# Performance work log

Hardware: AMD Instinct MI355X
Metric: run time of the kernel (lower is better)

## Reference

```python
import jax, jax.numpy as jnp
import numpy as np

K = 3  # == stride, neighbors per token


def setup_inputs() -> dict:
    key = jax.random.key(0)
    k1, k2, k3 = jax.random.split(key, 3)
    x = jax.random.normal(k1, (16, 64, 2048), dtype=jnp.float32)        # (B, C, T)
    W = jax.random.normal(k2, (64, 64, K), dtype=jnp.float32) * 0.05     # (O, I, K) conv1d weight
    b = jax.random.normal(k3, (64,), dtype=jnp.float32) * 0.05           # (O,) conv1d bias
    return {"x": x, "W": W, "b": b}


def reference(x, W, b):
    B, C, T = x.shape
    # pairwise squared euclidean distances over the channel dim: (B, T, T)
    nsq = jnp.sum(x * x, axis=1)                       # (B, T)
    dot = jnp.einsum('bct,bcs->bts', x, x)             # (B, T, T)
    dist = jnp.maximum(nsq[:, :, None] + nsq[:, None, :] - 2.0 * dot, 0.0)
    # K nearest neighbors (smallest distance -> top_k of negated dist)
    _, idx = jax.lax.top_k(-dist, K)                   # (B, T, K) int32 indices
    # gather neighbor features: prime[b, c, i*K + k] = x[b, c, idx[b, i, k]]
    idx_flat = idx.reshape(B, 1, T * K)
    prime = jnp.take_along_axis(x, jnp.broadcast_to(idx_flat, (B, C, T * K)), axis=2)
    # Conv1d with kernel_size=K, stride=K, padding=0 -> output length T
    out = jax.lax.conv_general_dilated(
        prime, W, window_strides=(K,), padding='VALID',
        dimension_numbers=('NCH', 'OIH', 'NCH'))
    return out + b[None, :, None]
```

## Files before the change

kernel.cpp:

```cpp
#include <hip/hip_runtime.h>

#define B_ 16
#define C_ 64
#define T_ 2048
#define O_ 64
#define KNN 3
#define HSPLIT 4
#define JCH (T_ / HSPLIT)

typedef short short8   __attribute__((ext_vector_type(8)));
typedef float f32x4    __attribute__((ext_vector_type(4)));
typedef unsigned short ushortx4 __attribute__((ext_vector_type(4)));

#define XT_OFF 0
#define XS_OFF (XT_OFF + B_ * T_ * C_)
#define NSQ_OFF (XS_OFF + B_ * T_ * C_)
#define WT_OFF (NSQ_OFF + B_ * T_)
#define CAND_OFF (WT_OFF + 192 * O_)

__device__ inline ushort bf16_rne(float f) {
    union { float f; unsigned u; } cv; cv.f = f;
    unsigned u = cv.u;
    u += 0x7FFF + ((u >> 16) & 1);
    return (ushort)(u >> 16);
}
__device__ inline float bf16_val(ushort h) {
    union { unsigned u; float f; } cv; cv.u = ((unsigned)h) << 16; return cv.f;
}

__global__ __launch_bounds__(256) void prep_kernel(const float* __restrict__ x,
                                                   const float* __restrict__ W,
                                                   float* __restrict__ ws) {
    float*  xT  = ws + XT_OFF;
    ushort* xs  = (ushort*)(ws + XS_OFF);
    float*  nsq = ws + NSQ_OFF;
    float*  Wt  = ws + WT_OFF;
    int blk = blockIdx.x;
    int tid = threadIdx.x;
    if (blk < B_ * (T_ / 64)) {
        int b  = blk / (T_ / 64);
        int t0 = (blk % (T_ / 64)) * 64;
        __shared__ float tl[64 * 65];
        #pragma unroll
        for (int r = 0; r < 16; ++r) {
            int e = r * 256 + tid;
            int c = e >> 6, t = e & 63;
            tl[c * 65 + t] = x[(b * C_ + c) * T_ + t0 + t];
        }
        __syncthreads();
        #pragma unroll
        for (int r = 0; r < 16; ++r) {
            int e = r * 256 + tid;
            int t = e >> 6, c = e & 63;
            float v = tl[c * 65 + t];
            size_t rowg = (size_t)(b * T_ + t0 + t);
            xT[rowg * 64 + c] = v;
            ushort hi = bf16_rne(v);
            float  fr = v - bf16_val(hi);
            ushort lo = bf16_rne(fr);
            xs[rowg * 128 + c]      = hi;
            xs[rowg * 128 + 64 + c] = lo;
        }
        if (tid < 64) {
            float s = 0.f;
            #pragma unroll
            for (int c = 0; c < 64; ++c) { float v = tl[c * 65 + tid]; s = fmaf(v, v, s); }
            nsq[b * T_ + t0 + tid] = s;
        }
    } else {
        int e = (blk - B_ * (T_ / 64)) * 256 + tid;
        if (e < O_ * C_ * KNN) {
            int o = e / (C_ * KNN);
            int c = (e / KNN) % C_;
            int k = e % KNN;
            Wt[(k * 64 + c) * O_ + o] = W[e];
        }
    }
}

__global__ __launch_bounds__(256, 4) void knn_mfma_kernel(const ushort* __restrict__ xs,
                                                          const float* __restrict__ nsq,
                                                          ushort* __restrict__ cand) {
    __shared__ __align__(16) ushort jbuf[2][32 * 128];
    __shared__ float nsqs[JCH];

    int bid = blockIdx.x;
    int g   = bid & 63;
    int m   = bid >> 6;
    int b   = g >> 2, h = g & 3;
    int i0  = m * 128;
    int tid = threadIdx.x;
    int w   = tid >> 6, l = tid & 63, lr = l & 15, lq = l >> 4;
    const ushort* xsb = xs + (size_t)b * T_ * 128;
    int jBase = h * JCH;

    if (tid < 128)
        ((float4*)nsqs)[tid] = ((const float4*)(nsq + b * T_ + jBase))[tid];

    short8 bA0, bA1, bA4, bA5, bB0, bB1, bB4, bB5;
    {
        const ushort* ia = xsb + (size_t)(i0 + w * 32 + lr) * 128 + lq * 8;
        bA0 = *(const short8*)(ia + 0);  bA1 = *(const short8*)(ia + 32);
        bA4 = *(const short8*)(ia + 64); bA5 = *(const short8*)(ia + 96);
        const ushort* ib2 = ia + 16 * 128;
        bB0 = *(const short8*)(ib2 + 0);  bB1 = *(const short8*)(ib2 + 32);
        bB4 = *(const short8*)(ib2 + 64); bB5 = *(const short8*)(ib2 + 96);
    }
    float niA = nsq[b * T_ + i0 + w * 32 + lr] + 4.0f;
    float niB = nsq[b * T_ + i0 + w * 32 + 16 + lr] + 4.0f;

    const float INF = __builtin_inff();
    float kA0 = INF, kA1 = INF, kA2 = INF, kA3 = INF;
    float kB0 = INF, kB1 = INF, kB2 = INF, kB3 = INF;

    int cSw = lr ^ (w * 4 + lq);
    #define ISSUE_DMA(jsv, bufv) {                                               \
        _Pragma("unroll")                                                        \
        for (int p = 0; p < 2; ++p) {                                            \
            int rloc = p * 16 + w * 4 + lq;                                      \
            const ushort* gp = xsb + (size_t)(jBase + (jsv) * 32 + rloc) * 128 + cSw * 8; \
            __builtin_amdgcn_global_load_lds(                                    \
                (const __attribute__((address_space(1))) void*)gp,               \
                (__attribute__((address_space(3))) void*)(jbuf[bufv] + (p * 16 + w * 4) * 128), \
                16, 0, 0);                                                       \
        } }

    ISSUE_DMA(0, 0);

    #pragma unroll 1
    for (int js = 0; js < 16; ++js) {
        asm volatile("s_waitcnt vmcnt(0)" ::: "memory");
        __syncthreads();
        if (js < 15) ISSUE_DMA(js + 1, (js + 1) & 1);
        const char* jb8 = (const char*)jbuf[js & 1];
        #pragma unroll
        for (int tile = 0; tile < 2; ++tile) {
            const char* rowp = jb8 + (tile * 16 + lr) * 256;
            short8 ah0 = *(const short8*)(rowp + ((( 0 + lq) ^ lr) << 4));
            short8 ah1 = *(const short8*)(rowp + ((( 4 + lq) ^ lr) << 4));
            short8 al0 = *(const short8*)(rowp + ((( 8 + lq) ^ lr) << 4));
            short8 al1 = *(const short8*)(rowp + (((12 + lq) ^ lr) << 4));
            f32x4 accA = {0.f, 0.f, 0.f, 0.f};
            f32x4 accB = {0.f, 0.f, 0.f, 0.f};
            accA = __builtin_amdgcn_mfma_f32_16x16x32_bf16(ah0, bA0, accA, 0, 0, 0);
            accB = __builtin_amdgcn_mfma_f32_16x16x32_bf16(ah0, bB0, accB, 0, 0, 0);
            accA = __builtin_amdgcn_mfma_f32_16x16x32_bf16(ah1, bA1, accA, 0, 0, 0);
            accB = __builtin_amdgcn_mfma_f32_16x16x32_bf16(ah1, bB1, accB, 0, 0, 0);
            accA = __builtin_amdgcn_mfma_f32_16x16x32_bf16(al0, bA0, accA, 0, 0, 0);
            accB = __builtin_amdgcn_mfma_f32_16x16x32_bf16(al0, bB0, accB, 0, 0, 0);
            accA = __builtin_amdgcn_mfma_f32_16x16x32_bf16(al1, bA1, accA, 0, 0, 0);
            accB = __builtin_amdgcn_mfma_f32_16x16x32_bf16(al1, bB1, accB, 0, 0, 0);
            accA = __builtin_amdgcn_mfma_f32_16x16x32_bf16(ah0, bA4, accA, 0, 0, 0);
            accB = __builtin_amdgcn_mfma_f32_16x16x32_bf16(ah0, bB4, accB, 0, 0, 0);
            accA = __builtin_amdgcn_mfma_f32_16x16x32_bf16(ah1, bA5, accA, 0, 0, 0);
            accB = __builtin_amdgcn_mfma_f32_16x16x32_bf16(ah1, bB5, accB, 0, 0, 0);
            float4 nv = *(const float4*)(nsqs + js * 32 + tile * 16 + lq * 4);
            int idb = ((js * 2 + tile) << 2) | (lq << 7);
            #define INS(K0, K1, K2, K3, sv, idv) {                                  \
                unsigned uu = (__float_as_uint(sv) & 0xFFFFFE00u) | (unsigned)(idv); \
                float kf = __uint_as_float(uu);                                      \
                float n0 = fminf(K0, kf);                                            \
                float n1 = __builtin_amdgcn_fmed3f(K0, K1, kf);                      \
                float n2 = __builtin_amdgcn_fmed3f(K1, K2, kf);                      \
                float n3 = __builtin_amdgcn_fmed3f(K2, K3, kf);                      \
                K0 = n0; K1 = n1; K2 = n2; K3 = n3; }
            {
                float s0 = fmaf(-2.f, accA[0], nv.x + niA); INS(kA0, kA1, kA2, kA3, s0, idb + 0);
                float s1 = fmaf(-2.f, accA[1], nv.y + niA); INS(kA0, kA1, kA2, kA3, s1, idb + 1);
                float s2 = fmaf(-2.f, accA[2], nv.z + niA); INS(kA0, kA1, kA2, kA3, s2, idb + 2);
                float s3 = fmaf(-2.f, accA[3], nv.w + niA); INS(kA0, kA1, kA2, kA3, s3, idb + 3);
            }
            {
                float s0 = fmaf(-2.f, accB[0], nv.x + niB); INS(kB0, kB1, kB2, kB3, s0, idb + 0);
                float s1 = fmaf(-2.f, accB[1], nv.y + niB); INS(kB0, kB1, kB2, kB3, s1, idb + 1);
                float s2 = fmaf(-2.f, accB[2], nv.z + niB); INS(kB0, kB1, kB2, kB3, s2, idb + 2);
                float s3 = fmaf(-2.f, accB[3], nv.w + niB); INS(kB0, kB1, kB2, kB3, s3, idb + 3);
            }
            #undef INS
        }
    }

    __syncthreads();
    float* fbuf = (float*)jbuf;
    {
        float* pa = fbuf + (w * 32 + lr) * 16 + lq * 4;
        pa[0] = kA0; pa[1] = kA1; pa[2] = kA2; pa[3] = kA3;
        float* pb = fbuf + (w * 32 + 16 + lr) * 16 + lq * 4;
        pb[0] = kB0; pb[1] = kB1; pb[2] = kB2; pb[3] = kB3;
    }
    __syncthreads();
    if (l < 32) {
        int rloc = w * 32 + l;
        const float* pr = fbuf + rloc * 16;
        float m0 = INF, m1 = INF, m2 = INF, m3 = INF;
        #pragma unroll
        for (int q2 = 0; q2 < 16; ++q2) {
            float kf = pr[q2];
            float n0 = fminf(m0, kf);
            float n1 = __builtin_amdgcn_fmed3f(m0, m1, kf);
            float n2 = __builtin_amdgcn_fmed3f(m1, m2, kf);
            float n3 = __builtin_amdgcn_fmed3f(m2, m3, kf);
            m0 = n0; m1 = n1; m2 = n2; m3 = n3;
        }
        ushortx4 cv;
        #define DEC(mf, slot) { unsigned u = __float_as_uint(mf) & 511u;             \
            cv[slot] = (ushort)(jBase + (((u & 127u) >> 2) << 4) + ((u >> 7) << 2) + (u & 3)); }
        DEC(m0, 0); DEC(m1, 1); DEC(m2, 2); DEC(m3, 3);
        #undef DEC
        int row = b * T_ + i0 + rloc;
        *(ushortx4*)(cand + (size_t)row * 16 + h * 4) = cv;
    }
}

__global__ __launch_bounds__(256) void refine_kernel(float* __restrict__ ws) {
    const float* xT  = ws + XT_OFF;
    const float* nsq = ws + NSQ_OFF;
    ushort* cand     = (ushort*)(ws + CAND_OFF);

    int tid = threadIdx.x;
    int w = tid >> 6, l = tid & 63, qw = l >> 4, lr = l & 15;
    int row = blockIdx.x * 16 + w * 4 + qw;
    int bT  = row & ~(T_ - 1);

    float4 av = *(const float4*)(xT + (size_t)row * 64 + lr * 4);
    int jown = cand[(size_t)row * 16 + lr];

    const float INF = __builtin_inff();
    float D0 = INF, D1 = INF, D2 = INF;
    int   I0 = 0x7FFFFFFF, I1 = 0x7FFFFFFF, I2 = 0x7FFFFFFF;

    #pragma unroll
    for (int t = 0; t < 16; ++t) {
        int jt = __shfl(jown, (l & 48) + t, 64);
        float4 bv = *(const float4*)(xT + (size_t)(bT + jt) * 64 + lr * 4);
        float p = fmaf(bv.w, av.w, fmaf(bv.z, av.z, fmaf(bv.y, av.y, bv.x * av.x)));
        p += __shfl_xor(p, 1, 64);
        p += __shfl_xor(p, 2, 64);
        p += __shfl_xor(p, 4, 64);
        p += __shfl_xor(p, 8, 64);
        float s = nsq[bT + jt] - 2.f * p;
        bool lt2 = (s < D2) || (s == D2 && jt < I2);
        bool lt1 = (s < D1) || (s == D1 && jt < I1);
        bool lt0 = (s < D0) || (s == D0 && jt < I0);
        float nD2 = lt1 ? D1 : (lt2 ? s : D2); int nI2 = lt1 ? I1 : (lt2 ? jt : I2);
        float nD1 = lt0 ? D0 : (lt1 ? s : D1); int nI1 = lt0 ? I0 : (lt1 ? jt : I1);
        D2 = nD2; I2 = nI2; D1 = nD1; I1 = nI1;
        D0 = lt0 ? s : D0; I0 = lt0 ? jt : I0;
    }
    if (lr == 0) {
        ushort* dst = cand + (size_t)row * 16;
        dst[0] = (ushort)I0; dst[1] = (ushort)I1; dst[2] = (ushort)I2;
    }
}

__global__ __launch_bounds__(256) void conv2_kernel(const float* __restrict__ ws,
                                                    const float* __restrict__ bias,
                                                    float* __restrict__ out) {
    const float*  xT   = ws + XT_OFF;
    const float*  Wt   = ws + WT_OFF;
    const ushort* cand = (const ushort*)(ws + CAND_OFF);

    __shared__ float g_s[192 * 32];

    int b   = blockIdx.x >> 6;
    int i0  = (blockIdx.x & 63) * 32;
    int tid = threadIdx.x;

    if (tid < 96) {
        int k  = tid >> 5;
        int ip = tid & 31;
        int j  = cand[(size_t)(b * T_ + i0 + ip) * 16 + k];
        const float4* src = (const float4*)(xT + ((size_t)b * T_ + j) * 64);
        #pragma unroll
        for (int c4 = 0; c4 < 16; ++c4) {
            float4 v = src[c4];
            int mm = k * 64 + c4 * 4;
            g_s[(mm + 0) * 32 + ip] = v.x;
            g_s[(mm + 1) * 32 + ip] = v.y;
            g_s[(mm + 2) * 32 + ip] = v.z;
            g_s[(mm + 3) * 32 + ip] = v.w;
        }
    }
    __syncthreads();

    int oq = tid >> 3;
    int iq = tid & 7;
    float a0x = 0.f, a0y = 0.f, a0z = 0.f, a0w = 0.f;
    float a1x = 0.f, a1y = 0.f, a1z = 0.f, a1w = 0.f;
    #pragma unroll 4
    for (int mm = 0; mm < 192; ++mm) {
        float2 wv = *(const float2*)(Wt + mm * 64 + oq * 2);
        float4 gv = *(const float4*)(g_s + mm * 32 + iq * 4);
        a0x = fmaf(wv.x, gv.x, a0x); a0y = fmaf(wv.x, gv.y, a0y);
        a0z = fmaf(wv.x, gv.z, a0z); a0w = fmaf(wv.x, gv.w, a0w);
        a1x = fmaf(wv.y, gv.x, a1x); a1y = fmaf(wv.y, gv.y, a1y);
        a1z = fmaf(wv.y, gv.z, a1z); a1w = fmaf(wv.y, gv.w, a1w);
    }
    int o0 = oq * 2;
    float b0 = bias[o0], b1 = bias[o0 + 1];
    float4 r0; r0.x = a0x + b0; r0.y = a0y + b0; r0.z = a0z + b0; r0.w = a0w + b0;
    float4 r1; r1.x = a1x + b1; r1.y = a1y + b1; r1.z = a1z + b1; r1.w = a1w + b1;
    *(float4*)(out + ((size_t)b * O_ + o0)     * T_ + i0 + iq * 4) = r0;
    *(float4*)(out + ((size_t)b * O_ + o0 + 1) * T_ + i0 + iq * 4) = r1;
}

extern "C" void kernel_launch(void* const* d_in, const int* in_sizes, int n_in,
                              void* d_out, int out_size, void* d_ws, size_t ws_size,
                              hipStream_t stream) {
    const float* x    = (const float*)d_in[0];
    const float* W    = (const float*)d_in[1];
    const float* bias = (const float*)d_in[2];
    float* out = (float*)d_out;
    float* ws  = (float*)d_ws;

    prep_kernel<<<B_ * (T_ / 64) + 48, 256, 0, stream>>>(x, W, ws);
    knn_mfma_kernel<<<1024, 256, 0, stream>>>(
        (const ushort*)(ws + XS_OFF), ws + NSQ_OFF, (ushort*)(ws + CAND_OFF));
    refine_kernel<<<B_ * T_ / 16, 256, 0, stream>>>(ws);
    conv2_kernel<<<B_ * 64, 256, 0, stream>>>(ws, bias, out);
}
```

Baseline: 142.1 us.

## Halve KNN column split and fuse refine into conv kernel

The KNN candidate kernel now splits the column range in two instead of four, doubling per-block loop length and halving the grid and the number of candidates per row from 16 to 8. Packed index bits grow by one, so the distance mantissa loses one more bit. The exact refine step is folded into the conv kernel, which stores the selected neighbors in shared memory, removing one launch and a global round trip. The conv output tiling changes to 4 outputs by 2 positions per thread. The risks are fewer blocks to fill the GPU, coarser approximate distances, and fewer candidates for the exact rerank.

```diff
diff --git a/kernel.cpp b/kernel.cpp
--- a/kernel.cpp
+++ b/kernel.cpp
@@ -5,7 +5,7 @@
 #define T_ 2048
 #define O_ 64
 #define KNN 3
-#define HSPLIT 4
+#define HSPLIT 2
 #define JCH (T_ / HSPLIT)
 
 typedef short short8   __attribute__((ext_vector_type(8)));
@@ -85,17 +85,16 @@
     __shared__ float nsqs[JCH];
 
     int bid = blockIdx.x;
-    int g   = bid & 63;
-    int m   = bid >> 6;
-    int b   = g >> 2, h = g & 3;
+    int g   = bid & 31;
+    int m   = bid >> 5;
+    int b   = g >> 1, h = g & 1;
     int i0  = m * 128;
     int tid = threadIdx.x;
     int w   = tid >> 6, l = tid & 63, lr = l & 15, lq = l >> 4;
     const ushort* xsb = xs + (size_t)b * T_ * 128;
     int jBase = h * JCH;
 
-    if (tid < 128)
-        ((float4*)nsqs)[tid] = ((const float4*)(nsq + b * T_ + jBase))[tid];
+    ((float4*)nsqs)[tid] = ((const float4*)(nsq + b * T_ + jBase))[tid];
 
     short8 bA0, bA1, bA4, bA5, bB0, bB1, bB4, bB5;
     {
@@ -128,10 +127,10 @@
     ISSUE_DMA(0, 0);
 
     #pragma unroll 1
-    for (int js = 0; js < 16; ++js) {
+    for (int js = 0; js < 32; ++js) {
         asm volatile("s_waitcnt vmcnt(0)" ::: "memory");
         __syncthreads();
-        if (js < 15) ISSUE_DMA(js + 1, (js + 1) & 1);
+        if (js < 31) ISSUE_DMA(js + 1, (js + 1) & 1);
         const char* jb8 = (const char*)jbuf[js & 1];
         #pragma unroll
         for (int tile = 0; tile < 2; ++tile) {
@@ -155,9 +154,9 @@
             accA = __builtin_amdgcn_mfma_f32_16x16x32_bf16(ah1, bA5, accA, 0, 0, 0);
             accB = __builtin_amdgcn_mfma_f32_16x16x32_bf16(ah1, bB5, accB, 0, 0, 0);
             float4 nv = *(const float4*)(nsqs + js * 32 + tile * 16 + lq * 4);
-            int idb = ((js * 2 + tile) << 2) | (lq << 7);
+            int idb = ((js * 2 + tile) << 2) | (lq << 8);
             #define INS(K0, K1, K2, K3, sv, idv) {                                  \
-                unsigned uu = (__float_as_uint(sv) & 0xFFFFFE00u) | (unsigned)(idv); \
+                unsigned uu = (__float_as_uint(sv) & 0xFFFFFC00u) | (unsigned)(idv); \
                 float kf = __uint_as_float(uu);                                      \
                 float n0 = fminf(K0, kf);                                            \
                 float n1 = __builtin_amdgcn_fmed3f(K0, K1, kf);                      \
@@ -203,74 +202,70 @@
             m0 = n0; m1 = n1; m2 = n2; m3 = n3;
         }
         ushortx4 cv;
-        #define DEC(mf, slot) { unsigned u = __float_as_uint(mf) & 511u;             \
-            cv[slot] = (ushort)(jBase + (((u & 127u) >> 2) << 4) + ((u >> 7) << 2) + (u & 3)); }
+        #define DEC(mf, slot) { unsigned u = __float_as_uint(mf) & 1023u;            \
+            cv[slot] = (ushort)(jBase + (((u >> 2) & 63u) << 4) + ((u >> 8) << 2) + (u & 3)); }
         DEC(m0, 0); DEC(m1, 1); DEC(m2, 2); DEC(m3, 3);
         #undef DEC
         int row = b * T_ + i0 + rloc;
-        *(ushortx4*)(cand + (size_t)row * 16 + h * 4) = cv;
-    }
-}
-
-__global__ __launch_bounds__(256) void refine_kernel(float* __restrict__ ws) {
-    const float* xT  = ws + XT_OFF;
-    const float* nsq = ws + NSQ_OFF;
-    ushort* cand     = (ushort*)(ws + CAND_OFF);
-
+        *(ushortx4*)(cand + (size_t)row * 8 + h * 4) = cv;
+    }
+}
+
+__global__ __launch_bounds__(256, 4) void conv_fused_kernel(const float* __restrict__ ws,
+                                                            const float* __restrict__ bias,
+                                                            float* __restrict__ out) {
+    const float*  xT   = ws + XT_OFF;
+    const float*  nsq  = ws + NSQ_OFF;
+    const float*  Wt   = ws + WT_OFF;
+    const ushort* cand = (const ushort*)(ws + CAND_OFF);
+
+    __shared__ float g_s[192 * 32];
+    __shared__ int   jsel3[32 * 3];
+
+    int bb  = blockIdx.x >> 6;
+    int i0  = (blockIdx.x & 63) * 32;
     int tid = threadIdx.x;
     int w = tid >> 6, l = tid & 63, qw = l >> 4, lr = l & 15;
-    int row = blockIdx.x * 16 + w * 4 + qw;
-    int bT  = row & ~(T_ - 1);
-
-    float4 av = *(const float4*)(xT + (size_t)row * 64 + lr * 4);
-    int jown = cand[(size_t)row * 16 + lr];
+    int bT = bb * T_;
 
     const float INF = __builtin_inff();
-    float D0 = INF, D1 = INF, D2 = INF;
-    int   I0 = 0x7FFFFFFF, I1 = 0x7FFFFFFF, I2 = 0x7FFFFFFF;
-
     #pragma unroll
-    for (int t = 0; t < 16; ++t) {
-        int jt = __shfl(jown, (l & 48) + t, 64);
-        float4 bv = *(const float4*)(xT + (size_t)(bT + jt) * 64 + lr * 4);
-        float p = fmaf(bv.w, av.w, fmaf(bv.z, av.z, fmaf(bv.y, av.y, bv.x * av.x)));
-        p += __shfl_xor(p, 1, 64);
-        p += __shfl_xor(p, 2, 64);
-        p += __shfl_xor(p, 4, 64);
-        p += __shfl_xor(p, 8, 64);
-        float s = nsq[bT + jt] - 2.f * p;
-        bool lt2 = (s < D2) || (s == D2 && jt < I2);
-        bool lt1 = (s < D1) || (s == D1 && jt < I1);
-        bool lt0 = (s < D0) || (s == D0 && jt < I0);
-        float nD2 = lt1 ? D1 : (lt2 ? s : D2); int nI2 = lt1 ? I1 : (lt2 ? jt : I2);
-        float nD1 = lt0 ? D0 : (lt1 ? s : D1); int nI1 = lt0 ? I0 : (lt1 ? jt : I1);
-        D2 = nD2; I2 = nI2; D1 = nD1; I1 = nI1;
-        D0 = lt0 ? s : D0; I0 = lt0 ? jt : I0;
-    }
-    if (lr == 0) {
-        ushort* dst = cand + (size_t)row * 16;
-        dst[0] = (ushort)I0; dst[1] = (ushort)I1; dst[2] = (ushort)I2;
-    }
-}
-
-__global__ __launch_bounds__(256) void conv2_kernel(const float* __restrict__ ws,
-                                                    const float* __restrict__ bias,
-                                                    float* __restrict__ out) {
-    const float*  xT   = ws + XT_OFF;
-    const float*  Wt   = ws + WT_OFF;
-    const ushort* cand = (const ushort*)(ws + CAND_OFF);
-
-    __shared__ float g_s[192 * 32];
-
-    int b   = blockIdx.x >> 6;
-    int i0  = (blockIdx.x & 63) * 32;
-    int tid = threadIdx.x;
+    for (int it = 0; it < 2; ++it) {
+        int rl  = w * 8 + it * 4 + qw;
+        int row = bT + i0 + rl;
+        float4 av = *(const float4*)(xT + (size_t)row * 64 + lr * 4);
+        int jown = cand[(size_t)row * 8 + (lr & 7)];
+        float D0 = INF, D1 = INF, D2 = INF;
+        int   I0 = 0x7FFFFFFF, I1 = 0x7FFFFFFF, I2 = 0x7FFFFFFF;
+        #pragma unroll
+        for (int t = 0; t < 8; ++t) {
+            int jt = __shfl(jown, (l & 48) + t, 64);
+            float4 bv = *(const float4*)(xT + (size_t)(bT + jt) * 64 + lr * 4);
+            float p = fmaf(bv.w, av.w, fmaf(bv.z, av.z, fmaf(bv.y, av.y, bv.x * av.x)));
+            p += __shfl_xor(p, 1, 64);
+            p += __shfl_xor(p, 2, 64);
+            p += __shfl_xor(p, 4, 64);
+            p += __shfl_xor(p, 8, 64);
+            float s = nsq[bT + jt] - 2.f * p;
+            bool lt2 = (s < D2) || (s == D2 && jt < I2);
+            bool lt1 = (s < D1) || (s == D1 && jt < I1);
+            bool lt0 = (s < D0) || (s == D0 && jt < I0);
+            float nD2 = lt1 ? D1 : (lt2 ? s : D2); int nI2 = lt1 ? I1 : (lt2 ? jt : I2);
+            float nD1 = lt0 ? D0 : (lt1 ? s : D1); int nI1 = lt0 ? I0 : (lt1 ? jt : I1);
+            D2 = nD2; I2 = nI2; D1 = nD1; I1 = nI1;
+            D0 = lt0 ? s : D0; I0 = lt0 ? jt : I0;
+        }
+        if (lr == 0) {
+            jsel3[rl * 3 + 0] = I0; jsel3[rl * 3 + 1] = I1; jsel3[rl * 3 + 2] = I2;
+        }
+    }
+    __syncthreads();
 
     if (tid < 96) {
         int k  = tid >> 5;
         int ip = tid & 31;
-        int j  = cand[(size_t)(b * T_ + i0 + ip) * 16 + k];
-        const float4* src = (const float4*)(xT + ((size_t)b * T_ + j) * 64);
+        int j  = jsel3[ip * 3 + k];
+        const float4* src = (const float4*)(xT + (size_t)(bT + j) * 64);
         #pragma unroll
         for (int c4 = 0; c4 < 16; ++c4) {
             float4 v = src[c4];
@@ -283,25 +278,30 @@
     }
     __syncthreads();
 
-    int oq = tid >> 3;
-    int iq = tid & 7;
-    float a0x = 0.f, a0y = 0.f, a0z = 0.f, a0w = 0.f;
-    float a1x = 0.f, a1y = 0.f, a1z = 0.f, a1w = 0.f;
+    int oq = tid >> 4;
+    int iq = tid & 15;
+    float a0x = 0.f, a0y = 0.f, a1x = 0.f, a1y = 0.f;
+    float a2x = 0.f, a2y = 0.f, a3x = 0.f, a3y = 0.f;
     #pragma unroll 4
     for (int mm = 0; mm < 192; ++mm) {
-        float2 wv = *(const float2*)(Wt + mm * 64 + oq * 2);
-        float4 gv = *(const float4*)(g_s + mm * 32 + iq * 4);
+        float4 wv = *(const float4*)(Wt + mm * 64 + oq * 4);
+        float2 gv = *(const float2*)(g_s + mm * 32 + iq * 2);
         a0x = fmaf(wv.x, gv.x, a0x); a0y = fmaf(wv.x, gv.y, a0y);
-        a0z = fmaf(wv.x, gv.z, a0z); a0w = fmaf(wv.x, gv.w, a0w);
         a1x = fmaf(wv.y, gv.x, a1x); a1y = fmaf(wv.y, gv.y, a1y);
-        a1z = fmaf(wv.y, gv.z, a1z); a1w = fmaf(wv.y, gv.w, a1w);
-    }
-    int o0 = oq * 2;
-    float b0 = bias[o0], b1 = bias[o0 + 1];
-    float4 r0; r0.x = a0x + b0; r0.y = a0y + b0; r0.z = a0z + b0; r0.w = a0w + b0;
-    float4 r1; r1.x = a1x + b1; r1.y = a1y + b1; r1.z = a1z + b1; r1.w = a1w + b1;
-    *(float4*)(out + ((size_t)b * O_ + o0)     * T_ + i0 + iq * 4) = r0;
-    *(float4*)(out + ((size_t)b * O_ + o0 + 1) * T_ + i0 + iq * 4) = r1;
+        a2x = fmaf(wv.z, gv.x, a2x); a2y = fmaf(wv.z, gv.y, a2y);
+        a3x = fmaf(wv.w, gv.x, a3x); a3y = fmaf(wv.w, gv.y, a3y);
+    }
+    int o0 = oq * 4;
+    float b0 = bias[o0], b1 = bias[o0 + 1], b2 = bias[o0 + 2], b3 = bias[o0 + 3];
+    float2 r0; r0.x = a0x + b0; r0.y = a0y + b0;
+    float2 r1; r1.x = a1x + b1; r1.y = a1y + b1;
+    float2 r2; r2.x = a2x + b2; r2.y = a2y + b2;
+    float2 r3; r3.x = a3x + b3; r3.y = a3y + b3;
+    size_t ob = (size_t)(bb * O_ + o0) * T_ + i0 + iq * 2;
+    *(float2*)(out + ob)          = r0;
+    *(float2*)(out + ob + T_)     = r1;
+    *(float2*)(out + ob + 2 * T_) = r2;
+    *(float2*)(out + ob + 3 * T_) = r3;
 }
 
 extern "C" void kernel_launch(void* const* d_in, const int* in_sizes, int n_in,
@@ -314,8 +314,7 @@
     float* ws  = (float*)d_ws;
 
     prep_kernel<<<B_ * (T_ / 64) + 48, 256, 0, stream>>>(x, W, ws);
-    knn_mfma_kernel<<<1024, 256, 0, stream>>>(
+    knn_mfma_kernel<<<512, 256, 0, stream>>>(
         (const ushort*)(ws + XS_OFF), ws + NSQ_OFF, (ushort*)(ws + CAND_OFF));
-    refine_kernel<<<B_ * T_ / 16, 256, 0, stream>>>(ws);
-    conv2_kernel<<<B_ * 64, 256, 0, stream>>>(ws, bias, out);
-}
+    conv_fused_kernel<<<B_ * 64, 256, 0, stream>>>(ws, bias, out);
+}
```

Result: no change. 139.6 us (-1.8%).
